# Kernel tuning notes

Hardware: AMD Instinct MI355X
Metric: run time of the kernel (lower is better)

The kernel has to match this reference:

```python
import jax, jax.numpy as jnp
import numpy as np

D_MODEL = 2048
D_INNER = 2048
N_QK = 32
N_V = 32
D_STATE = 64
D_CONV = 4
CHUNK = 128
CONV_DIM = D_INNER + 2 * N_QK * D_STATE  # 6144
IN_OUT = 2 * D_INNER + 2 * N_QK * D_STATE + N_V  # 8224


def setup_inputs() -> dict:
    key = jax.random.key(0)
    ks = jax.random.split(key, 6)
    u = jax.random.normal(ks[0], (2, 4096, D_MODEL), dtype=jnp.float32)
    W_in = jax.random.normal(ks[1], (IN_OUT, D_MODEL), dtype=jnp.float32) * 0.02
    conv_w = jax.random.normal(ks[2], (CONV_DIM, D_CONV), dtype=jnp.float32) * 0.2
    conv_b = jax.random.normal(ks[3], (CONV_DIM,), dtype=jnp.float32) * 0.02
    D = jnp.ones((N_V,), dtype=jnp.float32)
    z_bias = jnp.zeros((D_INNER,), dtype=jnp.float32)
    W_out = jax.random.normal(ks[4], (D_MODEL, D_INNER), dtype=jnp.float32) * 0.02
    return {"u": u, "W_in": W_in, "conv_w": conv_w, "conv_b": conv_b,
            "D": D, "z_bias": z_bias, "W_out": W_out}


def causal_depthwise_conv(x, w, b):
    # x: [B, L, C]; w: [C, K]; b: [C]. Torch Conv1d(groups=C, padding=K-1)[..., :L]
    B, L, C = x.shape
    K = w.shape[1]
    xp = jnp.pad(x, ((0, 0), (K - 1, 0), (0, 0)))
    y = b[None, None, :]
    for k in range(K):
        y = y + xp[:, k:k + L, :] * w[None, None, :, k]
    return y


def ssd_chunk_scan(x, dt, B, C, chunk):
    # Mamba2 SSD with A = -1 per head.
    # x: [b,l,h,p], dt: [b,l,h] (positive), B,C: [b,l,h,n]
    b, l, h, p = x.shape
    n = B.shape[-1]
    nc = l // chunk
    x = x.reshape(b, nc, chunk, h, p)
    dt = dt.reshape(b, nc, chunk, h)
    B = B.reshape(b, nc, chunk, h, n)
    C = C.reshape(b, nc, chunk, h, n)
    a = -dt                                  # A * dt
    cum = jnp.cumsum(a, axis=2)              # [b,nc,q,h]
    xdt = x * dt[..., None]                  # dt_t * x_t
    # ---- intra-chunk (causal, decay exp(cum_q - cum_k), q >= k) ----
    CB = jnp.einsum('bcqhn,bckhn->bchqk', C, B)
    cumT = jnp.swapaxes(cum, 2, 3)           # [b,nc,h,q]
    diff = cumT[..., :, None] - cumT[..., None, :]   # [b,nc,h,q,k]
    mask = jnp.tril(jnp.ones((chunk, chunk), dtype=bool))
    decay = jnp.exp(jnp.where(mask, diff, -jnp.inf))
    y_intra = jnp.einsum('bchqk,bckhp->bcqhp', CB * decay, xdt)
    # ---- per-chunk final states ----
    state_decay = jnp.exp(cum[:, :, -1:, :] - cum)   # [b,nc,q,h]
    states = jnp.einsum('bckhn,bckhp->bchpn', B * state_decay[..., None], xdt)
    chunk_decay = jnp.exp(cum[:, :, -1, :])          # [b,nc,h]
    # ---- inter-chunk recurrence ----
    def step(carry, inp):
        st, cd = inp  # st [b,h,p,n], cd [b,h]
        new = carry * cd[:, :, None, None] + st
        return new, carry  # emit the state *entering* this chunk
    init = jnp.zeros((b, h, p, n), dtype=x.dtype)
    _, prev = jax.lax.scan(step, init,
                           (jnp.moveaxis(states, 1, 0), jnp.moveaxis(chunk_decay, 1, 0)))
    prev = jnp.moveaxis(prev, 0, 1)                  # [b,nc,h,p,n]
    y_inter = jnp.einsum('bcqhn,bchpn->bcqhp', C * jnp.exp(cum)[..., None], prev)
    return (y_intra + y_inter).reshape(b, l, h, p)


def reference(u, W_in, conv_w, conv_b, D, z_bias, W_out):
    b, l, _ = u.shape  # l divisible by CHUNK (padded_len == l)
    xBCzA = jnp.einsum('bld,od->blo', u, W_in)
    xBC = xBCzA[..., :CONV_DIM]
    z = xBCzA[..., CONV_DIM:CONV_DIM + D_INNER]
    A_log = xBCzA[..., CONV_DIM + D_INNER:]
    xBC = causal_depthwise_conv(xBC, conv_w, conv_b)  # activation = identity
    x = xBC[..., :D_INNER]
    Bm = xBC[..., D_INNER:D_INNER + N_QK * D_STATE]
    Cm = xBC[..., D_INNER + N_QK * D_STATE:]
    x = x.reshape(b, l, N_V, D_INNER // N_V)
    Bm = Bm.reshape(b, l, N_QK, D_STATE)
    Cm = Cm.reshape(b, l, N_QK, D_STATE)
    dt = jax.nn.softplus(A_log)                       # [b,l,h]
    x_scan = x / dt[..., None]
    y = ssd_chunk_scan(x_scan, dt, Bm, Cm, CHUNK)
    y = y + D[None, None, :, None] * x                # Du uses undivided x
    y = y.reshape(b, l, D_INNER)
    out = jnp.einsum('bli,oi->blo', y * jax.nn.silu(z + z_bias), W_out)
    return out
```

## Files before the change

kernel.cpp:

```cpp
#include <hip/hip_runtime.h>
#include <math.h>

#define D_MODEL  2048
#define D_INNER  2048
#define N_QK     32
#define N_V      32
#define D_STATE  64
#define D_CONV   4
#define CHUNK    128
#define CONV_DIM 6144
#define IN_OUT   8224
#define BATCH    2
#define SEQ      4096
#define M_ROWS   (BATCH*SEQ)
#define NCHUNK   (SEQ/CHUNK)

typedef unsigned short bf16_t;
typedef __attribute__((ext_vector_type(4))) float f32x4;
typedef __attribute__((ext_vector_type(8))) short bf16x8;

#define SWZ64(r,c)  ((((r)*64)  + (c)) ^ (((r)&7)<<3))
#define SWZ128(r,c) ((((r)*128) + (c)) ^ (((r)&7)<<3))

__device__ __forceinline__ float b2f(bf16_t u) {
    union { unsigned int i; float f; } w; w.i = ((unsigned int)u) << 16; return w.f;
}
__device__ __forceinline__ bf16_t f2b(float f) {
    unsigned int x = __float_as_uint(f);
    return (bf16_t)((x + 0x7FFFu + ((x >> 16) & 1u)) >> 16);
}
__device__ __forceinline__ void store4b(bf16_t* dst, float4 v) {
    ushort4 u; u.x = f2b(v.x); u.y = f2b(v.y); u.z = f2b(v.z); u.w = f2b(v.w);
    *reinterpret_cast<ushort4*>(dst) = u;
}

__device__ __forceinline__ void gload_lds16(const bf16_t* g, bf16_t* l) {
    __builtin_amdgcn_global_load_lds((const __attribute__((address_space(1))) void*)g,
                                     (__attribute__((address_space(3))) void*)l,
                                     16, 0, 0);
}

__global__ __launch_bounds__(256) void f2b_kernel(const float* __restrict__ in,
                                                  bf16_t* __restrict__ out, long n)
{
    const long i = ((long)blockIdx.x * 256 + threadIdx.x) * 4;
    if (i < n) {
        float4 v = *reinterpret_cast<const float4*>(in + i);
        ushort4 o;
        o.x = f2b(v.x); o.y = f2b(v.y); o.z = f2b(v.z); o.w = f2b(v.w);
        *reinterpret_cast<ushort4*>(out + i) = o;
    }
}

template<int NTB, int K, bool OBF16>
__global__ __launch_bounds__(512, 2) void gemm256(const bf16_t* __restrict__ A,
                                                  const bf16_t* __restrict__ B,
                                                  void* __restrict__ Cv,
                                                  long ldc)
{
    constexpr int BK = 64;
    constexpr int NT = K / BK;
    __shared__ bf16_t As[2][2][8192];
    __shared__ bf16_t Bs[2][2][8192];

    const int nwg = gridDim.x;
    const int bid = blockIdx.x;
    const int wg  = ((nwg & 7) == 0) ? ((bid & 7) * (nwg >> 3) + (bid >> 3)) : bid;
    const int bm = (wg / NTB) * 256;
    const int bn = (wg % NTB) * 256;

    const int tid  = threadIdx.x;
    const int lane = tid & 63;
    const int wv   = tid >> 6;
    const int wr   = wv >> 2, wc = wv & 3;
    const int l15  = lane & 15, l4 = lane >> 4;

    f32x4 acc[8][4];
    #pragma unroll
    for (int i = 0; i < 8; ++i)
        #pragma unroll
        for (int j = 0; j < 4; ++j) acc[i][j] = (f32x4){0.f, 0.f, 0.f, 0.f};

    const bf16_t* Abase = A + (long)bm * K;
    const bf16_t* Bbase = B + (long)bn * K;

    auto stage_half = [&](int t, int buf, int kh) {
        #pragma unroll
        for (int it = 0; it < 2; ++it) {
            const int s   = it * 512 + tid;
            const int row = s >> 2;
            const int jp  = s & 3;
            const int jl  = jp ^ ((row >> 1) & 3);
            const long go = (long)row * K + t * BK + kh * 32 + jl * 8;
            gload_lds16(Abase + go, &As[buf][kh][s * 8]);
            gload_lds16(Bbase + go, &Bs[buf][kh][s * 8]);
        }
    };
    auto rdA = [&](int buf, int kh, int row) {
        const int jp = l4 ^ ((row >> 1) & 3);
        return *reinterpret_cast<const bf16x8*>(&As[buf][kh][(row * 4 + jp) * 8]);
    };
    auto rdB = [&](int buf, int kh, int row) {
        const int jp = l4 ^ ((row >> 1) & 3);
        return *reinterpret_cast<const bf16x8*>(&Bs[buf][kh][(row * 4 + jp) * 8]);
    };

    stage_half(0, 0, 0);
    stage_half(0, 0, 1);
    asm volatile("s_waitcnt vmcnt(4)" ::: "memory");
    __builtin_amdgcn_s_barrier();

    for (int t = 0; t < NT; ++t) {
        const int cur = t & 1;
        bf16x8 bfr[4], af[4];
        if (t + 1 < NT) stage_half(t + 1, cur ^ 1, 0);
        #pragma unroll
        for (int ni = 0; ni < 4; ++ni) bfr[ni] = rdB(cur, 0, wc * 64 + ni * 16 + l15);
        #pragma unroll
        for (int mi = 0; mi < 4; ++mi) af[mi] = rdA(cur, 0, wr * 128 + mi * 16 + l15);
        __builtin_amdgcn_s_setprio(1);
        #pragma unroll
        for (int mi = 0; mi < 4; ++mi)
            #pragma unroll
            for (int ni = 0; ni < 4; ++ni)
                acc[mi][ni] = __builtin_amdgcn_mfma_f32_16x16x32_bf16(
                    af[mi], bfr[ni], acc[mi][ni], 0, 0, 0);
        __builtin_amdgcn_s_setprio(0);
        __builtin_amdgcn_s_barrier();
        #pragma unroll
        for (int mi = 0; mi < 4; ++mi) af[mi] = rdA(cur, 0, wr * 128 + 64 + mi * 16 + l15);
        __builtin_amdgcn_s_setprio(1);
        #pragma unroll
        for (int mi = 0; mi < 4; ++mi)
            #pragma unroll
            for (int ni = 0; ni < 4; ++ni)
                acc[4 + mi][ni] = __builtin_amdgcn_mfma_f32_16x16x32_bf16(
                    af[mi], bfr[ni], acc[4 + mi][ni], 0, 0, 0);
        __builtin_amdgcn_s_setprio(0);
        if (t + 1 < NT) {
            stage_half(t + 1, cur ^ 1, 1);
            asm volatile("s_waitcnt vmcnt(8)" ::: "memory");
        } else {
            asm volatile("s_waitcnt vmcnt(0)" ::: "memory");
        }
        __builtin_amdgcn_s_barrier();
        #pragma unroll
        for (int ni = 0; ni < 4; ++ni) bfr[ni] = rdB(cur, 1, wc * 64 + ni * 16 + l15);
        #pragma unroll
        for (int mi = 0; mi < 4; ++mi) af[mi] = rdA(cur, 1, wr * 128 + mi * 16 + l15);
        __builtin_amdgcn_s_setprio(1);
        #pragma unroll
        for (int mi = 0; mi < 4; ++mi)
            #pragma unroll
            for (int ni = 0; ni < 4; ++ni)
                acc[mi][ni] = __builtin_amdgcn_mfma_f32_16x16x32_bf16(
                    af[mi], bfr[ni], acc[mi][ni], 0, 0, 0);
        __builtin_amdgcn_s_setprio(0);
        __builtin_amdgcn_s_barrier();
        #pragma unroll
        for (int mi = 0; mi < 4; ++mi) af[mi] = rdA(cur, 1, wr * 128 + 64 + mi * 16 + l15);
        __builtin_amdgcn_s_setprio(1);
        #pragma unroll
        for (int mi = 0; mi < 4; ++mi)
            #pragma unroll
            for (int ni = 0; ni < 4; ++ni)
                acc[4 + mi][ni] = __builtin_amdgcn_mfma_f32_16x16x32_bf16(
                    af[mi], bfr[ni], acc[4 + mi][ni], 0, 0, 0);
        __builtin_amdgcn_s_setprio(0);
        if (t + 1 < NT) { asm volatile("s_waitcnt vmcnt(4)" ::: "memory"); }
        __builtin_amdgcn_s_barrier();
    }

    #pragma unroll
    for (int mf = 0; mf < 8; ++mf) {
        const long grow0 = bm + wr * 128 + mf * 16 + l4 * 4;
        #pragma unroll
        for (int ni = 0; ni < 4; ++ni) {
            const int gcol = bn + wc * 64 + ni * 16 + l15;
            #pragma unroll
            for (int j = 0; j < 4; ++j) {
                if (OBF16)
                    ((bf16_t*)Cv)[(grow0 + j) * ldc + gcol] = f2b(acc[mf][ni][j]);
                else
                    ((float*)Cv)[(grow0 + j) * ldc + gcol] = acc[mf][ni][j];
            }
        }
    }
}

template<int N, int K, bool OBF16>
__global__ __launch_bounds__(256) void gemm_mfma(const bf16_t* __restrict__ A,
                                                 const bf16_t* __restrict__ B,
                                                 void* __restrict__ Cv,
                                                 long ldc)
{
    constexpr int BM = 128, BN = 128, BK = 64;
    constexpr int NTB = (N + BN - 1) / BN;
    __shared__ bf16_t As[BM * BK];
    __shared__ bf16_t Bs[BM * BK];

    const int nwg = gridDim.x;
    const int bid = blockIdx.x;
    const int wg  = ((nwg & 7) == 0) ? ((bid & 7) * (nwg >> 3) + (bid >> 3)) : bid;
    const int bm = (wg / NTB) * BM;
    const int bn = (wg % NTB) * BN;

    const int tid  = threadIdx.x;
    const int lane = tid & 63;
    const int wv   = tid >> 6;
    const int wr   = wv >> 1, wc = wv & 1;

    f32x4 acc[4][4];
    #pragma unroll
    for (int i = 0; i < 4; ++i)
        #pragma unroll
        for (int j = 0; j < 4; ++j) acc[i][j] = (f32x4){0.f, 0.f, 0.f, 0.f};

    for (int k0 = 0; k0 < K; k0 += BK) {
        #pragma unroll
        for (int it = 0; it < 4; ++it) {
            const int seg = it * 256 + tid;
            const int row = seg >> 3, c16 = seg & 7;
            gload_lds16(A + (long)(bm + row) * K + k0 + c16 * 8,
                        &As[row * BK + c16 * 8]);
            int brow = bn + row;
            if constexpr (N % BN != 0) brow = min(brow, N - 1);
            gload_lds16(B + (long)brow * K + k0 + c16 * 8,
                        &Bs[row * BK + c16 * 8]);
        }
        __syncthreads();
        #pragma unroll
        for (int kk = 0; kk < 2; ++kk) {
            bf16x8 af[4], bfr[4];
            const int kc = kk * 32 + (lane >> 4) * 8;
            #pragma unroll
            for (int mi = 0; mi < 4; ++mi) {
                const int row = wr * 64 + mi * 16 + (lane & 15);
                af[mi] = *reinterpret_cast<const bf16x8*>(&As[row * BK + kc]);
            }
            #pragma unroll
            for (int ni = 0; ni < 4; ++ni) {
                const int row = wc * 64 + ni * 16 + (lane & 15);
                bfr[ni] = *reinterpret_cast<const bf16x8*>(&Bs[row * BK + kc]);
            }
            #pragma unroll
            for (int mi = 0; mi < 4; ++mi)
                #pragma unroll
                for (int ni = 0; ni < 4; ++ni)
                    acc[mi][ni] = __builtin_amdgcn_mfma_f32_16x16x32_bf16(
                        af[mi], bfr[ni], acc[mi][ni], 0, 0, 0);
        }
        __syncthreads();
    }

    #pragma unroll
    for (int mi = 0; mi < 4; ++mi) {
        const long row0 = bm + wr * 64 + mi * 16 + ((lane >> 4) << 2);
        #pragma unroll
        for (int ni = 0; ni < 4; ++ni) {
            const int col = bn + wc * 64 + ni * 16 + (lane & 15);
            if (N % BN != 0 && col >= N) continue;
            #pragma unroll
            for (int j = 0; j < 4; ++j) {
                if (OBF16)
                    ((bf16_t*)Cv)[(row0 + j) * ldc + col] = f2b(acc[mi][ni][j]);
                else
                    ((float*)Cv)[(row0 + j) * ldc + col] = acc[mi][ni][j];
            }
        }
    }
}

__device__ __forceinline__ float4 conv4v(const bf16_t* __restrict__ xb, long m, int l,
                                         int col, const float* __restrict__ cw,
                                         const float* __restrict__ cbv)
{
    float4 acc = *reinterpret_cast<const float4*>(cbv + col);
    float4 wc0 = *reinterpret_cast<const float4*>(cw + (long)col * 4);
    float4 wc1 = *reinterpret_cast<const float4*>(cw + (long)col * 4 + 4);
    float4 wc2 = *reinterpret_cast<const float4*>(cw + (long)col * 4 + 8);
    float4 wc3 = *reinterpret_cast<const float4*>(cw + (long)col * 4 + 12);
    const float t0[4] = {wc0.x, wc0.y, wc0.z, wc0.w};
    const float t1[4] = {wc1.x, wc1.y, wc1.z, wc1.w};
    const float t2[4] = {wc2.x, wc2.y, wc2.z, wc2.w};
    const float t3[4] = {wc3.x, wc3.y, wc3.z, wc3.w};
    #pragma unroll
    for (int tap = 0; tap < 4; ++tap) {
        if (l - 3 + tap < 0) continue;
        const bf16_t* p = xb + (m - 3 + tap) * (long)IN_OUT + col;
        ushort4 v = *reinterpret_cast<const ushort4*>(p);
        acc.x = fmaf(b2f(v.x), t0[tap], acc.x);
        acc.y = fmaf(b2f(v.y), t1[tap], acc.y);
        acc.z = fmaf(b2f(v.z), t2[tap], acc.z);
        acc.w = fmaf(b2f(v.w), t3[tap], acc.w);
    }
    return acc;
}

__global__ __launch_bounds__(256) void ssd_states(const bf16_t* __restrict__ xb,
                                                  const float* __restrict__ cw,
                                                  const float* __restrict__ cbv,
                                                  float* __restrict__ states,
                                                  float* __restrict__ cumbuf,
                                                  float* __restrict__ cdecay)
{
    const int h = blockIdx.x, c = blockIdx.y, b = blockIdx.z;
    __shared__ bf16_t sx [128 * 64];
    __shared__ bf16_t sBr[128 * 64];
    __shared__ bf16_t sXT[64 * 128];
    __shared__ bf16_t sBT[64 * 128];
    __shared__ float  cum[CHUNK];
    const int t = threadIdx.x;
    const long mbase = (long)b * SEQ + (long)c * CHUNK;
    const long cb = ((long)b * NCHUNK + c) * N_QK + h;

    if (t < CHUNK) {
        const float a = b2f(xb[(mbase + t) * (long)IN_OUT + (CONV_DIM + D_INNER) + h]);
        cum[t] = -((a > 20.f) ? a : log1pf(expf(a)));
    }
    for (int idx = t; idx < CHUNK * 16; idx += 256) {
        const int k = idx >> 4, q4 = (idx & 15) * 4;
        const long m = mbase + k;
        const int l = (int)(m & (SEQ - 1));
        float4 xv = conv4v(xb, m, l, h * 64 + q4, cw, cbv);
        float4 bv = conv4v(xb, m, l, D_INNER + h * 64 + q4, cw, cbv);
        store4b(&sx [SWZ64(k, q4)], xv);
        store4b(&sBr[SWZ64(k, q4)], bv);
    }
    __syncthreads();
    #pragma unroll
    for (int s = 1; s < CHUNK; s <<= 1) {
        float pv = 0.f;
        if (t < CHUNK && t >= s) pv = cum[t - s];
        __syncthreads();
        if (t < CHUNK && t >= s) cum[t] += pv;
        __syncthreads();
    }
    const float clast = cum[CHUNK - 1];
    {
        const int j = t & 127;
        const int c8b = (t >> 7) * 4;
        const float ej = __expf(clast - cum[j]);
        #pragma unroll
        for (int it = 0; it < 4; ++it) {
            const int c8 = c8b + it;
            bf16x8 xv = *reinterpret_cast<const bf16x8*>(&sx [SWZ64(j, c8 * 8)]);
            bf16x8 bv = *reinterpret_cast<const bf16x8*>(&sBr[SWZ64(j, c8 * 8)]);
            #pragma unroll
            for (int e = 0; e < 8; ++e) {
                sXT[SWZ128(c8 * 8 + e, j)] = xv[e];
                sBT[SWZ128(c8 * 8 + e, j)] = f2b(b2f((bf16_t)bv[e]) * ej);
            }
        }
    }
    __syncthreads();

    const int lane = t & 63, wv = t >> 6;
    const int l15 = lane & 15, l4 = lane >> 4;
    f32x4 acc[4];
    #pragma unroll
    for (int nj = 0; nj < 4; ++nj) acc[nj] = (f32x4){0.f, 0.f, 0.f, 0.f};
    #pragma unroll
    for (int ks = 0; ks < 4; ++ks) {
        const int kc = ks * 32 + l4 * 8;
        bf16x8 af = *reinterpret_cast<const bf16x8*>(&sXT[SWZ128(wv * 16 + l15, kc)]);
        #pragma unroll
        for (int nj = 0; nj < 4; ++nj) {
            bf16x8 bf = *reinterpret_cast<const bf16x8*>(&sBT[SWZ128(nj * 16 + l15, kc)]);
            acc[nj] = __builtin_amdgcn_mfma_f32_16x16x32_bf16(af, bf, acc[nj], 0, 0, 0);
        }
    }
    #pragma unroll
    for (int nj = 0; nj < 4; ++nj) {
        #pragma unroll
        for (int jj = 0; jj < 4; ++jj) {
            const int p = wv * 16 + l4 * 4 + jj;
            states[cb * 4096 + (long)p * 64 + nj * 16 + l15] = acc[nj][jj];
        }
    }
    if (t < CHUNK) cumbuf[cb * CHUNK + t] = cum[t];
    if (t == 0)   cdecay[cb] = __expf(clast);
}

__global__ __launch_bounds__(256) void ssd_scan(float* __restrict__ states,
                                                const float* __restrict__ cdecay)
{
    const int bid = blockIdx.x;
    const int bh = bid >> 2, q = bid & 3;
    const int b = bh >> 5, h = bh & 31;
    const int t = threadIdx.x;
    const int off = q * 1024 + t * 4;
    float4 carry = make_float4(0.f, 0.f, 0.f, 0.f);
    for (int c = 0; c < NCHUNK; ++c) {
        const long cb = ((long)b * NCHUNK + c) * N_QK + h;
        const long base = cb * 4096 + off;
        const float cd = cdecay[cb];
        float4 st = *reinterpret_cast<const float4*>(&states[base]);
        *reinterpret_cast<float4*>(&states[base]) = carry;
        carry.x = fmaf(carry.x, cd, st.x);
        carry.y = fmaf(carry.y, cd, st.y);
        carry.z = fmaf(carry.z, cd, st.z);
        carry.w = fmaf(carry.w, cd, st.w);
    }
}

__global__ __launch_bounds__(256) void ssd_out(const bf16_t* __restrict__ xb,
                                               const float* __restrict__ cumbuf,
                                               const float* __restrict__ prevst,
                                               const float* __restrict__ Dvec,
                                               const float* __restrict__ zbias,
                                               const float* __restrict__ cw,
                                               const float* __restrict__ cbv,
                                               bf16_t* __restrict__ yz)
{
    const int h = blockIdx.x, c = blockIdx.y, b = blockIdx.z;
    __shared__ bf16_t sC[128 * 64];
    __shared__ bf16_t sB[128 * 64];
    __shared__ bf16_t sXQ[128 * 64];
    __shared__ bf16_t sXT[64 * 128];
    __shared__ bf16_t sP[64 * 64];
    __shared__ float  cum[CHUNK];
    const int t = threadIdx.x;
    const long mbase = (long)b * SEQ + (long)c * CHUNK;
    const long cb = ((long)b * NCHUNK + c) * N_QK + h;
    if (t < CHUNK) cum[t] = cumbuf[cb * CHUNK + t];
    for (int idx = t; idx < CHUNK * 16; idx += 256) {
        const int k = idx >> 4, q4 = (idx & 15) * 4;
        const long m = mbase + k;
        const int l = (int)(m & (SEQ - 1));
        float4 xv = conv4v(xb, m, l, h * 64 + q4, cw, cbv);
        float4 bv = conv4v(xb, m, l, D_INNER + h * 64 + q4, cw, cbv);
        float4 cv = conv4v(xb, m, l, 2 * D_INNER + h * 64 + q4, cw, cbv);
        store4b(&sXQ[SWZ64(k, q4)], xv);
        store4b(&sB [SWZ64(k, q4)], bv);
        store4b(&sC [SWZ64(k, q4)], cv);
    }
    for (int idx = t; idx < 64 * 16; idx += 256) {
        const int p = idx >> 4, q4 = (idx & 15) * 4;
        float4 v = *reinterpret_cast<const float4*>(prevst + cb * 4096 + p * 64 + q4);
        store4b(&sP[SWZ64(p, q4)], v);
    }
    __syncthreads();
    {
        const int j = t & 127;
        const int c8b = (t >> 7) * 4;
        #pragma unroll
        for (int it = 0; it < 4; ++it) {
            const int c8 = c8b + it;
            bf16x8 v = *reinterpret_cast<const bf16x8*>(&sXQ[SWZ64(j, c8 * 8)]);
            #pragma unroll
            for (int e = 0; e < 8; ++e) sXT[SWZ128(c8 * 8 + e, j)] = v[e];
        }
    }
    __syncthreads();

    const int lane = t & 63, wv = t >> 6;
    const int w32 = wv * 32, l15 = lane & 15, l4 = lane >> 4;
    bf16_t* sQ = sXQ;

    f32x4 yac[2][4], iac[2][4];
    #pragma unroll
    for (int mi = 0; mi < 2; ++mi)
        #pragma unroll
        for (int np = 0; np < 4; ++np) {
            yac[mi][np] = (f32x4){0.f, 0.f, 0.f, 0.f};
            iac[mi][np] = (f32x4){0.f, 0.f, 0.f, 0.f};
        }

    #pragma unroll
    for (int H = 0; H < 2; ++H) {
        if (H == 1 && wv < 2) break;
        const int j0 = H * 64;
        f32x4 sac[2][4];
        #pragma unroll
        for (int mi = 0; mi < 2; ++mi)
            #pragma unroll
            for (int nj = 0; nj < 4; ++nj) sac[mi][nj] = (f32x4){0.f, 0.f, 0.f, 0.f};
        #pragma unroll
        for (int kk = 0; kk < 2; ++kk) {
            const int kc = kk * 32 + l4 * 8;
            bf16x8 af0 = *reinterpret_cast<const bf16x8*>(&sC[SWZ64(w32 + l15, kc)]);
            bf16x8 af1 = *reinterpret_cast<const bf16x8*>(&sC[SWZ64(w32 + 16 + l15, kc)]);
            #pragma unroll
            for (int nj = 0; nj < 4; ++nj) {
                bf16x8 bfj = *reinterpret_cast<const bf16x8*>(&sB[SWZ64(j0 + nj * 16 + l15, kc)]);
                if (j0 + nj * 16 <= w32 + 15)
                    sac[0][nj] = __builtin_amdgcn_mfma_f32_16x16x32_bf16(af0, bfj, sac[0][nj], 0, 0, 0);
                if (j0 + nj * 16 <= w32 + 31)
                    sac[1][nj] = __builtin_amdgcn_mfma_f32_16x16x32_bf16(af1, bfj, sac[1][nj], 0, 0, 0);
            }
        }
        #pragma unroll
        for (int mi = 0; mi < 2; ++mi) {
            #pragma unroll
            for (int nj = 0; nj < 4; ++nj) {
                const int jcol = nj * 16 + l15;
                const int jg = j0 + jcol;
                #pragma unroll
                for (int jj = 0; jj < 4; ++jj) {
                    const int i = w32 + mi * 16 + l4 * 4 + jj;
                    const float q = (jg <= i) ? __expf(cum[i] - cum[jg]) * sac[mi][nj][jj] : 0.f;
                    sQ[SWZ64(i, jcol)] = f2b(q);
                }
            }
        }
        #pragma unroll
        for (int kk = 0; kk < 2; ++kk) {
            const int kc = kk * 32 + l4 * 8;
            bf16x8 qa0 = *reinterpret_cast<const bf16x8*>(&sQ[SWZ64(w32 + l15, kc)]);
            bf16x8 qa1 = *reinterpret_cast<const bf16x8*>(&sQ[SWZ64(w32 + 16 + l15, kc)]);
            #pragma unroll
            for (int np = 0; np < 4; ++np) {
                bf16x8 xf = *reinterpret_cast<const bf16x8*>(&sXT[SWZ128(np * 16 + l15, j0 + kc)]);
                yac[0][np] = __builtin_amdgcn_mfma_f32_16x16x32_bf16(qa0, xf, yac[0][np], 0, 0, 0);
                yac[1][np] = __builtin_amdgcn_mfma_f32_16x16x32_bf16(qa1, xf, yac[1][np], 0, 0, 0);
            }
        }
    }
    #pragma unroll
    for (int kk = 0; kk < 2; ++kk) {
        const int kc = kk * 32 + l4 * 8;
        bf16x8 cf0 = *reinterpret_cast<const bf16x8*>(&sC[SWZ64(w32 + l15, kc)]);
        bf16x8 cf1 = *reinterpret_cast<const bf16x8*>(&sC[SWZ64(w32 + 16 + l15, kc)]);
        #pragma unroll
        for (int np = 0; np < 4; ++np) {
            bf16x8 pf = *reinterpret_cast<const bf16x8*>(&sP[SWZ64(np * 16 + l15, kc)]);
            iac[0][np] = __builtin_amdgcn_mfma_f32_16x16x32_bf16(cf0, pf, iac[0][np], 0, 0, 0);
            iac[1][np] = __builtin_amdgcn_mfma_f32_16x16x32_bf16(cf1, pf, iac[1][np], 0, 0, 0);
        }
    }
    const float dh = Dvec[h];
    #pragma unroll
    for (int mi = 0; mi < 2; ++mi) {
        #pragma unroll
        for (int jj = 0; jj < 4; ++jj) {
            const int i = w32 + mi * 16 + l4 * 4 + jj;
            const float ei = __expf(cum[i]);
            const long m = mbase + i;
            const bf16_t* zr = xb + m * (long)IN_OUT + CONV_DIM + h * 64;
            bf16_t* orow = yz + m * (long)D_INNER + h * 64;
            #pragma unroll
            for (int np = 0; np < 4; ++np) {
                const int p = np * 16 + l15;
                const float xval = b2f(sXT[SWZ128(p, i)]);
                const float y = yac[mi][np][jj] + ei * iac[mi][np][jj] + dh * xval;
                const float zv = b2f(zr[p]) + zbias[h * 64 + p];
                const float s = zv / (1.f + __expf(-zv));
                orow[p] = f2b(y * s);
            }
        }
    }
}

extern "C" void kernel_launch(void* const* d_in, const int* in_sizes, int n_in,
                              void* d_out, int out_size, void* d_ws, size_t ws_size,
                              hipStream_t stream)
{
    const float* u      = (const float*)d_in[0];
    const float* W_in   = (const float*)d_in[1];
    const float* conv_w = (const float*)d_in[2];
    const float* conv_b = (const float*)d_in[3];
    const float* Dv     = (const float*)d_in[4];
    const float* z_bias = (const float*)d_in[5];
    const float* W_out  = (const float*)d_in[6];
    float* out = (float*)d_out;

    char* w = (char*)d_ws;
    bf16_t* xbcza = (bf16_t*)w;  w += (long)M_ROWS * IN_OUT * 2;
    bf16_t* wob   = (bf16_t*)w;  w += (long)2048 * 2048 * 2;
    char* ureg = w;
    bf16_t* ub  = (bf16_t*)ureg;
    bf16_t* wib = (bf16_t*)(ureg + (long)M_ROWS * D_MODEL * 2);
    bf16_t* yzb = (bf16_t*)ureg;
    float*  cumb   = (float*)(ureg + (long)M_ROWS * D_INNER * 2);
    float*  states = cumb + (long)BATCH * NCHUNK * N_QK * CHUNK;
    float*  cdec   = states + (long)BATCH * NCHUNK * N_QK * 4096;

    f2b_kernel<<<(int)(((long)M_ROWS * D_MODEL / 4 + 255) / 256), 256, 0, stream>>>(
        u, ub, (long)M_ROWS * D_MODEL);
    f2b_kernel<<<(int)(((long)IN_OUT * D_MODEL / 4 + 255) / 256), 256, 0, stream>>>(
        W_in, wib, (long)IN_OUT * D_MODEL);
    f2b_kernel<<<(int)(((long)D_MODEL * D_INNER / 4 + 255) / 256), 256, 0, stream>>>(
        W_out, wob, (long)D_MODEL * D_INNER);

    gemm256<32, D_MODEL, true><<<(M_ROWS / 256) * 32, 512, 0, stream>>>(
        ub, wib, xbcza, IN_OUT);
    gemm_mfma<32, D_MODEL, true><<<(M_ROWS / 128), 256, 0, stream>>>(
        ub, wib + (long)8192 * D_MODEL, xbcza + 8192, IN_OUT);

    ssd_states<<<dim3(N_QK, NCHUNK, BATCH), 256, 0, stream>>>(xbcza, conv_w, conv_b,
                                                              states, cumb, cdec);

    ssd_scan<<<BATCH * N_QK * 4, 256, 0, stream>>>(states, cdec);

    ssd_out<<<dim3(N_QK, NCHUNK, BATCH), 256, 0, stream>>>(xbcza, cumb, states, Dv, z_bias,
                                                           conv_w, conv_b, yzb);

    gemm256<8, D_INNER, false><<<(M_ROWS / 256) * 8, 512, 0, stream>>>(
        yzb, wob, out, D_MODEL);
}
```

Before: 830.6 us.

## Store SSD chunk states in bf16, use wave-shuffle cumsum, reorder in-proj GEMM tiles

Chunk states are now written as swizzled bf16 instead of fp32. This halves state traffic through the states, scan and out kernels and lets ssd_out load them straight into LDS with async global-to-LDS copies. The per-chunk cumulative sum of dt is now a wave-level shuffle scan instead of a barrier-heavy LDS scan. The input-projection GEMM maps workgroups N-major for a different L2 reuse pattern. The cost is bf16 rounding of the inter-chunk states and of the scan inputs and outputs, which may reduce accuracy.

```diff
diff --git a/kernel.cpp b/kernel.cpp
--- a/kernel.cpp
+++ b/kernel.cpp
@@ -52,7 +52,7 @@
     }
 }
 
-template<int NTB, int K, bool OBF16>
+template<int NTB, int K, bool OBF16, bool BNMAJOR>
 __global__ __launch_bounds__(512, 2) void gemm256(const bf16_t* __restrict__ A,
                                                   const bf16_t* __restrict__ B,
                                                   void* __restrict__ Cv,
@@ -66,8 +66,9 @@
     const int nwg = gridDim.x;
     const int bid = blockIdx.x;
     const int wg  = ((nwg & 7) == 0) ? ((bid & 7) * (nwg >> 3) + (bid >> 3)) : bid;
-    const int bm = (wg / NTB) * 256;
-    const int bn = (wg % NTB) * 256;
+    int bm, bn;
+    if (BNMAJOR) { bm = (wg & 31) * 256; bn = (wg >> 5) * 256; }
+    else         { bm = (wg / NTB) * 256; bn = (wg % NTB) * 256; }
 
     const int tid  = threadIdx.x;
     const int lane = tid & 63;
@@ -300,7 +301,7 @@
 __global__ __launch_bounds__(256) void ssd_states(const bf16_t* __restrict__ xb,
                                                   const float* __restrict__ cw,
                                                   const float* __restrict__ cbv,
-                                                  float* __restrict__ states,
+                                                  bf16_t* __restrict__ states,
                                                   float* __restrict__ cumbuf,
                                                   float* __restrict__ cdecay)
 {
@@ -310,13 +311,21 @@
     __shared__ bf16_t sXT[64 * 128];
     __shared__ bf16_t sBT[64 * 128];
     __shared__ float  cum[CHUNK];
+    __shared__ float  w0tot;
     const int t = threadIdx.x;
     const long mbase = (long)b * SEQ + (long)c * CHUNK;
     const long cb = ((long)b * NCHUNK + c) * N_QK + h;
 
+    float v = 0.f;
     if (t < CHUNK) {
         const float a = b2f(xb[(mbase + t) * (long)IN_OUT + (CONV_DIM + D_INNER) + h]);
-        cum[t] = -((a > 20.f) ? a : log1pf(expf(a)));
+        v = -((a > 20.f) ? a : log1pf(expf(a)));
+        #pragma unroll
+        for (int s = 1; s < 64; s <<= 1) {
+            const float u2 = __shfl_up(v, s, 64);
+            if ((t & 63) >= s) v += u2;
+        }
+        if (t == 63) w0tot = v;
     }
     for (int idx = t; idx < CHUNK * 16; idx += 256) {
         const int k = idx >> 4, q4 = (idx & 15) * 4;
@@ -328,14 +337,9 @@
         store4b(&sBr[SWZ64(k, q4)], bv);
     }
     __syncthreads();
-    #pragma unroll
-    for (int s = 1; s < CHUNK; s <<= 1) {
-        float pv = 0.f;
-        if (t < CHUNK && t >= s) pv = cum[t - s];
-        __syncthreads();
-        if (t < CHUNK && t >= s) cum[t] += pv;
-        __syncthreads();
-    }
+    if (t >= 64 && t < CHUNK) v += w0tot;
+    if (t < CHUNK) cum[t] = v;
+    __syncthreads();
     const float clast = cum[CHUNK - 1];
     {
         const int j = t & 127;
@@ -375,14 +379,14 @@
         #pragma unroll
         for (int jj = 0; jj < 4; ++jj) {
             const int p = wv * 16 + l4 * 4 + jj;
-            states[cb * 4096 + (long)p * 64 + nj * 16 + l15] = acc[nj][jj];
+            states[cb * 4096 + SWZ64(p, nj * 16 + l15)] = f2b(acc[nj][jj]);
         }
     }
     if (t < CHUNK) cumbuf[cb * CHUNK + t] = cum[t];
     if (t == 0)   cdecay[cb] = __expf(clast);
 }
 
-__global__ __launch_bounds__(256) void ssd_scan(float* __restrict__ states,
+__global__ __launch_bounds__(256) void ssd_scan(bf16_t* __restrict__ states,
                                                 const float* __restrict__ cdecay)
 {
     const int bid = blockIdx.x;
@@ -393,20 +397,23 @@
     float4 carry = make_float4(0.f, 0.f, 0.f, 0.f);
     for (int c = 0; c < NCHUNK; ++c) {
         const long cb = ((long)b * NCHUNK + c) * N_QK + h;
-        const long base = cb * 4096 + off;
+        bf16_t* p = states + cb * 4096 + off;
         const float cd = cdecay[cb];
-        float4 st = *reinterpret_cast<const float4*>(&states[base]);
-        *reinterpret_cast<float4*>(&states[base]) = carry;
-        carry.x = fmaf(carry.x, cd, st.x);
-        carry.y = fmaf(carry.y, cd, st.y);
-        carry.z = fmaf(carry.z, cd, st.z);
-        carry.w = fmaf(carry.w, cd, st.w);
+        ushort4 su = *reinterpret_cast<const ushort4*>(p);
+        ushort4 pv;
+        pv.x = f2b(carry.x); pv.y = f2b(carry.y);
+        pv.z = f2b(carry.z); pv.w = f2b(carry.w);
+        *reinterpret_cast<ushort4*>(p) = pv;
+        carry.x = fmaf(carry.x, cd, b2f(su.x));
+        carry.y = fmaf(carry.y, cd, b2f(su.y));
+        carry.z = fmaf(carry.z, cd, b2f(su.z));
+        carry.w = fmaf(carry.w, cd, b2f(su.w));
     }
 }
 
 __global__ __launch_bounds__(256) void ssd_out(const bf16_t* __restrict__ xb,
                                                const float* __restrict__ cumbuf,
-                                               const float* __restrict__ prevst,
+                                               const bf16_t* __restrict__ prevst,
                                                const float* __restrict__ Dvec,
                                                const float* __restrict__ zbias,
                                                const float* __restrict__ cw,
@@ -424,6 +431,11 @@
     const long mbase = (long)b * SEQ + (long)c * CHUNK;
     const long cb = ((long)b * NCHUNK + c) * N_QK + h;
     if (t < CHUNK) cum[t] = cumbuf[cb * CHUNK + t];
+    #pragma unroll
+    for (int it = 0; it < 2; ++it) {
+        const int s = it * 256 + t;
+        gload_lds16(prevst + cb * 4096 + s * 8, &sP[s * 8]);
+    }
     for (int idx = t; idx < CHUNK * 16; idx += 256) {
         const int k = idx >> 4, q4 = (idx & 15) * 4;
         const long m = mbase + k;
@@ -435,11 +447,6 @@
         store4b(&sB [SWZ64(k, q4)], bv);
         store4b(&sC [SWZ64(k, q4)], cv);
     }
-    for (int idx = t; idx < 64 * 16; idx += 256) {
-        const int p = idx >> 4, q4 = (idx & 15) * 4;
-        float4 v = *reinterpret_cast<const float4*>(prevst + cb * 4096 + p * 64 + q4);
-        store4b(&sP[SWZ64(p, q4)], v);
-    }
     __syncthreads();
     {
         const int j = t & 127;
@@ -573,8 +580,8 @@
     bf16_t* wib = (bf16_t*)(ureg + (long)M_ROWS * D_MODEL * 2);
     bf16_t* yzb = (bf16_t*)ureg;
     float*  cumb   = (float*)(ureg + (long)M_ROWS * D_INNER * 2);
-    float*  states = cumb + (long)BATCH * NCHUNK * N_QK * CHUNK;
-    float*  cdec   = states + (long)BATCH * NCHUNK * N_QK * 4096;
+    bf16_t* states = (bf16_t*)(cumb + (long)BATCH * NCHUNK * N_QK * CHUNK);
+    float*  cdec   = (float*)(states + (long)BATCH * NCHUNK * N_QK * 4096);
 
     f2b_kernel<<<(int)(((long)M_ROWS * D_MODEL / 4 + 255) / 256), 256, 0, stream>>>(
         u, ub, (long)M_ROWS * D_MODEL);
@@ -583,7 +590,7 @@
     f2b_kernel<<<(int)(((long)D_MODEL * D_INNER / 4 + 255) / 256), 256, 0, stream>>>(
         W_out, wob, (long)D_MODEL * D_INNER);
 
-    gemm256<32, D_MODEL, true><<<(M_ROWS / 256) * 32, 512, 0, stream>>>(
+    gemm256<32, D_MODEL, true, true><<<(M_ROWS / 256) * 32, 512, 0, stream>>>(
         ub, wib, xbcza, IN_OUT);
     gemm_mfma<32, D_MODEL, true><<<(M_ROWS / 128), 256, 0, stream>>>(
         ub, wib + (long)8192 * D_MODEL, xbcza + 8192, IN_OUT);
@@ -596,6 +603,6 @@
     ssd_out<<<dim3(N_QK, NCHUNK, BATCH), 256, 0, stream>>>(xbcza, cumb, states, Dv, z_bias,
                                                            conv_w, conv_b, yzb);
 
-    gemm256<8, D_INNER, false><<<(M_ROWS / 256) * 8, 512, 0, stream>>>(
+    gemm256<8, D_INNER, false, false><<<(M_ROWS / 256) * 8, 512, 0, stream>>>(
         yzb, wob, out, D_MODEL);
 }
```

After: 839.4 us. About the same (+1.1%).
